# Kernel tuning notes

Hardware: AMD Instinct MI355X
Metric: run time of the kernel (lower is better)

Reference implementation:

```python
import itertools
import jax, jax.numpy as jnp
import numpy as np

# ---- constant tables / bases ----
Y_TABLE_NP = np.array([
    [16, 11, 10, 16, 24, 40, 51, 61],
    [12, 12, 14, 19, 26, 58, 60, 55],
    [14, 13, 16, 24, 40, 57, 69, 56],
    [14, 17, 22, 29, 51, 87, 80, 62],
    [18, 22, 37, 56, 68, 109, 103, 77],
    [24, 35, 55, 64, 81, 104, 113, 92],
    [49, 64, 78, 87, 103, 121, 120, 101],
    [72, 92, 95, 98, 112, 100, 103, 99]], dtype=np.float32)
C_TABLE_NP = np.full((8, 8), 99, dtype=np.float32)
C_TABLE_NP[:4, :4] = np.array([[17, 18, 24, 47], [18, 21, 26, 66],
                               [24, 26, 56, 99], [47, 66, 99, 99]], dtype=np.float32)

def _bases():
    dct = np.zeros((8, 8, 8, 8), dtype=np.float32)
    idct = np.zeros((8, 8, 8, 8), dtype=np.float32)
    for x, y, u, v in itertools.product(range(8), repeat=4):
        dct[x, y, u, v] = np.cos((2 * x + 1) * u * np.pi / 16) * np.cos((2 * y + 1) * v * np.pi / 16)
        idct[x, y, u, v] = np.cos((2 * u + 1) * x * np.pi / 16) * np.cos((2 * v + 1) * y * np.pi / 16)
    alpha = np.array([1.0 / np.sqrt(2)] + [1.0] * 7, dtype=np.float32)
    ao = np.outer(alpha, alpha).astype(np.float32)
    return jnp.asarray(dct), jnp.asarray(ao * 0.25), jnp.asarray(idct), jnp.asarray(ao)

DCT_T, DCT_SCALE, IDCT_T, ALPHA = _bases()
FACTOR = 0.4  # quality_to_factor(80) = (200 - 2*80)/100


def diff_round(x):
    r = jnp.round(x)
    return r + (x - r) ** 3


def _blocks(img):  # (B,H,W) -> (B, H*W/64, 8, 8)
    B, H, W = img.shape
    return img.reshape(B, H // 8, 8, W // 8, 8).transpose(0, 1, 3, 2, 4).reshape(B, -1, 8, 8)


def _merge(patches, H, W):  # (B, N, 8, 8) -> (B, H, W)
    B = patches.shape[0]
    return patches.reshape(B, H // 8, W // 8, 8, 8).transpose(0, 1, 3, 2, 4).reshape(B, H, W)


def setup_inputs() -> dict:
    key = jax.random.key(0)
    image = jax.random.uniform(key, (32, 3, 512, 512), dtype=jnp.float32)
    return {"image": image,
            "y_table": jnp.asarray(Y_TABLE_NP),
            "c_table": jnp.asarray(C_TABLE_NP)}


def reference(image, y_table, c_table):
    B, _, H, W = image.shape
    x = image * 255.0
    # RGB -> YCbCr (matrix stored transposed in torch, tensordot over channel)
    rgb2ycc = jnp.array([[0.299, 0.587, 0.114],
                         [-0.168736, -0.331264, 0.5],
                         [0.5, -0.418688, -0.081312]], dtype=jnp.float32)
    shift = jnp.array([0.0, 128.0, 128.0], dtype=jnp.float32)
    ycc = jnp.einsum('bchw,kc->bhwk', x, rgb2ycc) + shift  # (B,H,W,3)
    y = ycc[..., 0]
    # chroma subsampling: 2x2 average pool
    def pool2(ch):
        return ch.reshape(B, H // 2, 2, W // 2, 2).mean(axis=(2, 4))
    cb = pool2(ycc[..., 1])
    cr = pool2(ycc[..., 2])

    def compress(ch, table):
        blk = _blocks(ch) - 128.0
        d = DCT_SCALE * jnp.einsum('bnxy,xyuv->bnuv', blk, DCT_T)
        return diff_round(d / (table * FACTOR))

    yq = compress(y, y_table)
    cbq = compress(cb, c_table)
    crq = compress(cr, c_table)

    def decompress(q, table, h, w):
        d = (q * (table * FACTOR)) * ALPHA
        blk = 0.25 * jnp.einsum('bnuv,uvxy->bnxy', d, IDCT_T) + 128.0
        return _merge(blk, h, w)

    y_rec = decompress(yq, y_table, H, W)
    cb_rec = decompress(cbq, c_table, H // 2, W // 2)
    cr_rec = decompress(crq, c_table, H // 2, W // 2)

    def up2(ch):
        b, h, w = ch.shape
        return jnp.broadcast_to(ch[:, :, None, :, None], (b, h, 2, w, 2)).reshape(b, 2 * h, 2 * w)

    ycc_rec = jnp.stack([y_rec, up2(cb_rec), up2(cr_rec)], axis=-1)  # (B,H,W,3)
    ycc2rgb = jnp.array([[1.0, 0.0, 1.402],
                         [1.0, -0.344136, -0.714136],
                         [1.0, 1.772, 0.0]], dtype=jnp.float32)
    shift2 = jnp.array([0.0, -128.0, -128.0], dtype=jnp.float32)
    rgb = jnp.einsum('bhwk,ck->bhwc', ycc_rec + shift2, ycc2rgb)
    rgb = rgb.transpose(0, 3, 1, 2)  # (B,3,H,W)
    return jnp.clip(rgb, 0.0, 255.0) / 255.0
```

## Files before the change

### kernel.cpp

```cpp
#include <hip/hip_runtime.h>
#include <math.h>

#define IMG_H 512
#define IMG_W 512
#define IMG_HW (IMG_H * IMG_W)

namespace {

constexpr float CFv[9] = {
    1.0f,
    0.98078528040323044913f,
    0.92387953251128675613f,
    0.83146961230254523708f,
    0.70710678118654752440f,
    0.55557023301960222474f,
    0.38268343236508977173f,
    0.19509032201612826785f,
    0.0f
};

struct CTab {
    float  cf[8][8];
    double cd[8][8];
    float  aof[8][8];
    float  scalef[8][8];
};

constexpr CTab make_ctab() {
    CTab t{};
    for (int y = 0; y < 8; y++) {
        for (int v = 0; v < 8; v++) {
            int a = ((2 * y + 1) * v) & 31;
            if (a > 16) a = 32 - a;
            float val = (a <= 8) ? CFv[a] : -CFv[16 - a];
            t.cf[y][v] = val;
            t.cd[y][v] = (double)val;
        }
    }
    constexpr float A0 = 0.70710678118654752440f;
    for (int u = 0; u < 8; u++) {
        for (int v = 0; v < 8; v++) {
            float au = (u == 0) ? A0 : 1.0f;
            float av = (v == 0) ? A0 : 1.0f;
            float ao = au * av;
            t.aof[u][v] = ao;
            t.scalef[u][v] = ao * 0.25f;
        }
    }
    return t;
}

constexpr CTab CT = make_ctab();

#define OFF_CBP 8448
#define OFF_CRP 10624
#define OFF_QY  12800
#define OFF_QC  13952
#define SMEM_BYTES 15104

__device__ __forceinline__ void xpose8_d(double v[8]) {
    const int l = threadIdx.x & 7;
    #pragma unroll
    for (int m = 1; m < 8; m <<= 1) {
        #pragma unroll
        for (int k = 0; k < 8; k++) {
            if ((k & m) == 0) {
                const int kp = k | m;
                double send = (l & m) ? v[k] : v[kp];
                double recv = __shfl_xor(send, m);
                v[k]  = (l & m) ? recv : v[k];
                v[kp] = (l & m) ? v[kp] : recv;
            }
        }
    }
}

__device__ __forceinline__ void xpose8_f(float v[8]) {
    const int l = threadIdx.x & 7;
    #pragma unroll
    for (int m = 1; m < 8; m <<= 1) {
        #pragma unroll
        for (int k = 0; k < 8; k++) {
            if ((k & m) == 0) {
                const int kp = k | m;
                float send = (l & m) ? v[k] : v[kp];
                float recv = __shfl_xor(send, m);
                v[k]  = (l & m) ? recv : v[k];
                v[kp] = (l & m) ? v[kp] : recv;
            }
        }
    }
}

}

__global__ void __launch_bounds__(256, 6) djpeg_kernel(
    const float* __restrict__ img,
    const float* __restrict__ ytab,
    const float* __restrict__ ctab,
    float* __restrict__ out)
{
    __shared__ __align__(16) unsigned char smem[SMEM_BYTES];
    double* lY  = (double*)(smem);
    double* cbP = (double*)(smem + OFF_CBP);
    double* crP = (double*)(smem + OFF_CRP);
    double* qY  = (double*)(smem + OFF_QY);
    double* qC  = (double*)(smem + OFF_QC);
    float* yR  = (float*)(smem);
    float* cbR = (float*)(smem + 4224);
    float* crR = (float*)(smem + 5312);

    const int t  = threadIdx.x;
    const int X0 = blockIdx.x * 64;
    const int Y0 = blockIdx.y * 16;
    const int bi = blockIdx.z;

    if (t < 128) {
        const float* tab = (t < 64) ? ytab : ctab;
        double* q = (t < 64) ? qY : qC;
        int e = t & 63, u = e >> 3, v = e & 7;
        float tfacf = tab[e] * 0.4f;
        double tf = (double)tfacf;
        q[v * 18 + 2 * u]     = (double)CT.scalef[u][v] / tf;
        q[v * 18 + 2 * u + 1] = tf * (double)CT.aof[u][v];
    }

    {
        const int x = t & 63, yb = t >> 6;
        double accb[2] = {0.0, 0.0}, accr[2] = {0.0, 0.0};
        size_t base = ((size_t)bi * 3) * IMG_HW + (size_t)Y0 * IMG_W + X0 + x;
        #pragma unroll
        for (int i = 0; i < 4; i++) {
            int y = yb * 4 + i;
            size_t p = base + (size_t)y * IMG_W;
            double R = (double)img[p] * 255.0;
            double G = (double)img[p + IMG_HW] * 255.0;
            double B = (double)img[p + 2 * IMG_HW] * 255.0;
            double Yv = (double)0.299f * R + (double)0.587f * G + (double)0.114f * B;
            double Cb = -(double)0.168736f * R - (double)0.331264f * G + (double)0.5f * B + 128.0;
            double Cr = (double)0.5f * R - (double)0.418688f * G - (double)0.081312f * B + 128.0;
            lY[y * 66 + x] = Yv;
            accb[i >> 1] += Cb;
            accr[i >> 1] += Cr;
        }
        #pragma unroll
        for (int p2 = 0; p2 < 2; p2++) {
            double hb = accb[p2] + __shfl_xor(accb[p2], 1);
            double hr = accr[p2] + __shfl_xor(accr[p2], 1);
            if ((x & 1) == 0) {
                int pr = yb * 2 + p2;
                cbP[pr * 34 + (x >> 1)] = hb * 0.25;
                crP[pr * 34 + (x >> 1)] = hr * 0.25;
            }
        }
    }
    __syncthreads();

    const bool act = (t < 192);
    const int r = t & 7;
    const double* src = lY;
    const double* qtab = qY;
    float* dstR = yR;
    if (act) {
        if (t < 128) {
            int g = t >> 3, by = g >> 3, bx = g & 7;
            src  = lY + (by * 8 + r) * 66 + bx * 8;
            dstR = yR + (by * 8 + r) * 66 + bx * 8;
            qtab = qY;
        } else {
            int c = t - 128;
            int isCr = c >> 5;
            int g2 = (c >> 3) & 3;
            src  = (isCr ? crP : cbP) + r * 34 + g2 * 8;
            dstR = (isCr ? crR : cbR) + r * 34 + g2 * 8;
            qtab = qC;
        }
    }

    double s1[8];
    if (act) {
        double a[8];
        #pragma unroll
        for (int y = 0; y < 8; y++) a[y] = src[y] - 128.0;
        #pragma unroll
        for (int v = 0; v < 8; v++) {
            double s = a[0] * CT.cd[0][v];
            #pragma unroll
            for (int y = 1; y < 8; y++) s += a[y] * CT.cd[y][v];
            s1[v] = s;
        }
        xpose8_d(s1);
    }

    float mrow[8];
    if (act) {
        float dq[8];
        #pragma unroll
        for (int u = 0; u < 8; u++) {
            double D = s1[0] * CT.cd[0][u];
            #pragma unroll
            for (int x = 1; x < 8; x++) D += s1[x] * CT.cd[x][u];
            double fs = qtab[r * 18 + 2 * u];
            double ds = qtab[r * 18 + 2 * u + 1];
            double xq = D * fs;
            double rq = rint(xq);
            double e  = xq - rq;
            dq[u] = (float)((rq + e * e * e) * ds);
        }
        #pragma unroll
        for (int x = 0; x < 8; x++) {
            float s = dq[0] * CT.cf[x][0];
            #pragma unroll
            for (int u = 1; u < 8; u++) s += dq[u] * CT.cf[x][u];
            mrow[x] = s;
        }
        xpose8_f(mrow);
    }

    __syncthreads();

    if (act) {
        #pragma unroll
        for (int y = 0; y < 8; y++) {
            float s = mrow[0] * CT.cf[y][0];
            #pragma unroll
            for (int v = 1; v < 8; v++) s += mrow[v] * CT.cf[y][v];
            dstR[y] = 0.25f * s + 128.0f;
        }
    }
    __syncthreads();

    {
        const int x = t & 63, yb = t >> 6;
        size_t base = ((size_t)bi * 3) * IMG_HW + (size_t)Y0 * IMG_W + X0 + x;
        #pragma unroll
        for (int i = 0; i < 4; i++) {
            int y = yb * 4 + i;
            float Yv = yR[y * 66 + x];
            float Cb = cbR[(y >> 1) * 34 + (x >> 1)] - 128.0f;
            float Cr = crR[(y >> 1) * 34 + (x >> 1)] - 128.0f;
            float Rr = Yv + 1.402f * Cr;
            float Gg = Yv - 0.344136f * Cb - 0.714136f * Cr;
            float Bb = Yv + 1.772f * Cb;
            Rr = fminf(fmaxf(Rr, 0.0f), 255.0f) * (1.0f / 255.0f);
            Gg = fminf(fmaxf(Gg, 0.0f), 255.0f) * (1.0f / 255.0f);
            Bb = fminf(fmaxf(Bb, 0.0f), 255.0f) * (1.0f / 255.0f);
            size_t p = base + (size_t)y * IMG_W;
            out[p] = Rr;
            out[p + IMG_HW] = Gg;
            out[p + 2 * IMG_HW] = Bb;
        }
    }
}

extern "C" void kernel_launch(void* const* d_in, const int* in_sizes, int n_in,
                              void* d_out, int out_size, void* d_ws, size_t ws_size,
                              hipStream_t stream) {
    (void)n_in; (void)out_size; (void)d_ws; (void)ws_size;
    const float* img = (const float*)d_in[0];
    const float* yt  = (const float*)d_in[1];
    const float* ct  = (const float*)d_in[2];
    float* out = (float*)d_out;
    int B = in_sizes[0] / (3 * IMG_HW);
    dim3 grid(IMG_W / 64, IMG_H / 16, B);
    djpeg_kernel<<<grid, dim3(256, 1, 1), 0, stream>>>(img, yt, ct, out);
}
```

Baseline: 183.5 us.

## Use butterfly DCT/IDCT, LDS transposes, and float4 vectorized global I/O

Replaces the naive 8x8 matrix-product DCT and IDCT with even/odd butterfly factorizations, cutting double-precision multiplies. Replaces the shuffle-based register transposes with transposes through shared memory. Switches global loads and stores and the LDS staging to float4/double2 vector accesses, with pitches changed to keep alignment. Part of the dequantization and cube rounding now runs in float instead of double, which trades some precision for cheaper arithmetic.

```diff
diff --git a/kernel.cpp b/kernel.cpp
--- a/kernel.cpp
+++ b/kernel.cpp
@@ -52,47 +52,48 @@
 
 constexpr CTab CT = make_ctab();
 
+__device__ __forceinline__ void fwd8_d(const double a[8], double s[8]) {
+    double e0 = a[0] + a[7], e1 = a[1] + a[6], e2 = a[2] + a[5], e3 = a[3] + a[4];
+    double o0 = a[0] - a[7], o1 = a[1] - a[6], o2 = a[2] - a[5], o3 = a[3] - a[4];
+    double ee0 = e0 + e3, ee1 = e1 + e2, eo0 = e0 - e3, eo1 = e1 - e2;
+    s[0] = ee0 + ee1;
+    s[4] = (ee0 - ee1) * CT.cd[0][4];
+    s[2] = eo0 * CT.cd[0][2] + eo1 * CT.cd[1][2];
+    s[6] = eo0 * CT.cd[0][6] + eo1 * CT.cd[1][6];
+    #pragma unroll
+    for (int k = 0; k < 4; k++) {
+        const int v = 2 * k + 1;
+        s[v] = o0 * CT.cd[0][v] + o1 * CT.cd[1][v] + o2 * CT.cd[2][v] + o3 * CT.cd[3][v];
+    }
+}
+
+__device__ __forceinline__ void inv8_f(const float d[8], float m[8]) {
+    float eea = fmaf(CT.cf[0][4], d[4], d[0]);
+    float eeb = fmaf(CT.cf[1][4], d[4], d[0]);
+    float u2a = d[2] * CT.cf[0][2] + d[6] * CT.cf[0][6];
+    float u2b = d[2] * CT.cf[1][2] + d[6] * CT.cf[1][6];
+    float E0 = eea + u2a, E1 = eeb + u2b, E2 = eeb - u2b, E3 = eea - u2a;
+    float O0 = d[1] * CT.cf[0][1] + d[3] * CT.cf[0][3] + d[5] * CT.cf[0][5] + d[7] * CT.cf[0][7];
+    float O1 = d[1] * CT.cf[1][1] + d[3] * CT.cf[1][3] + d[5] * CT.cf[1][5] + d[7] * CT.cf[1][7];
+    float O2 = d[1] * CT.cf[2][1] + d[3] * CT.cf[2][3] + d[5] * CT.cf[2][5] + d[7] * CT.cf[2][7];
+    float O3 = d[1] * CT.cf[3][1] + d[3] * CT.cf[3][3] + d[5] * CT.cf[3][5] + d[7] * CT.cf[3][7];
+    m[0] = E0 + O0; m[7] = E0 - O0;
+    m[1] = E1 + O1; m[6] = E1 - O1;
+    m[2] = E2 + O2; m[5] = E2 - O2;
+    m[3] = E3 + O3; m[4] = E3 - O3;
+}
+
+}
+
 #define OFF_CBP 8448
 #define OFF_CRP 10624
-#define OFF_QY  12800
-#define OFF_QC  13952
-#define SMEM_BYTES 15104
-
-__device__ __forceinline__ void xpose8_d(double v[8]) {
-    const int l = threadIdx.x & 7;
-    #pragma unroll
-    for (int m = 1; m < 8; m <<= 1) {
-        #pragma unroll
-        for (int k = 0; k < 8; k++) {
-            if ((k & m) == 0) {
-                const int kp = k | m;
-                double send = (l & m) ? v[k] : v[kp];
-                double recv = __shfl_xor(send, m);
-                v[k]  = (l & m) ? recv : v[k];
-                v[kp] = (l & m) ? v[kp] : recv;
-            }
-        }
-    }
-}
-
-__device__ __forceinline__ void xpose8_f(float v[8]) {
-    const int l = threadIdx.x & 7;
-    #pragma unroll
-    for (int m = 1; m < 8; m <<= 1) {
-        #pragma unroll
-        for (int k = 0; k < 8; k++) {
-            if ((k & m) == 0) {
-                const int kp = k | m;
-                float send = (l & m) ? v[k] : v[kp];
-                float recv = __shfl_xor(send, m);
-                v[k]  = (l & m) ? recv : v[k];
-                v[kp] = (l & m) ? v[kp] : recv;
-            }
-        }
-    }
-}
-
-}
+#define OFF_QYF 12800
+#define OFF_QCF 13440
+#define OFF_DSY 14080
+#define OFF_DSC 14464
+#define OFF_CBR 4352
+#define OFF_CRR 5504
+#define SMEM_BYTES 14848
 
 __global__ void __launch_bounds__(256, 6) djpeg_kernel(
     const float* __restrict__ img,
@@ -101,14 +102,16 @@
     float* __restrict__ out)
 {
     __shared__ __align__(16) unsigned char smem[SMEM_BYTES];
-    double* lY  = (double*)(smem);
-    double* cbP = (double*)(smem + OFF_CBP);
-    double* crP = (double*)(smem + OFF_CRP);
-    double* qY  = (double*)(smem + OFF_QY);
-    double* qC  = (double*)(smem + OFF_QC);
-    float* yR  = (float*)(smem);
-    float* cbR = (float*)(smem + 4224);
-    float* crR = (float*)(smem + 5312);
+    double* lY   = (double*)(smem);
+    double* cbP  = (double*)(smem + OFF_CBP);
+    double* crP  = (double*)(smem + OFF_CRP);
+    double* qYfs = (double*)(smem + OFF_QYF);
+    double* qCfs = (double*)(smem + OFF_QCF);
+    float*  dsY  = (float*)(smem + OFF_DSY);
+    float*  dsC  = (float*)(smem + OFF_DSC);
+    float*  yR   = (float*)(smem);
+    float*  cbR  = (float*)(smem + OFF_CBR);
+    float*  crR  = (float*)(smem + OFF_CRR);
 
     const int t  = threadIdx.x;
     const int X0 = blockIdx.x * 64;
@@ -117,139 +120,158 @@
 
     if (t < 128) {
         const float* tab = (t < 64) ? ytab : ctab;
-        double* q = (t < 64) ? qY : qC;
+        double* qf = (t < 64) ? qYfs : qCfs;
+        float*  df = (t < 64) ? dsY : dsC;
         int e = t & 63, u = e >> 3, v = e & 7;
         float tfacf = tab[e] * 0.4f;
         double tf = (double)tfacf;
-        q[v * 18 + 2 * u]     = (double)CT.scalef[u][v] / tf;
-        q[v * 18 + 2 * u + 1] = tf * (double)CT.aof[u][v];
+        qf[v * 10 + u] = (double)CT.scalef[u][v] / tf;
+        df[v * 12 + u] = (float)(tf * (double)CT.aof[u][v]);
     }
 
     {
-        const int x = t & 63, yb = t >> 6;
-        double accb[2] = {0.0, 0.0}, accr[2] = {0.0, 0.0};
-        size_t base = ((size_t)bi * 3) * IMG_HW + (size_t)Y0 * IMG_W + X0 + x;
+        const int xq = t & 15, yb = t >> 4;
+        size_t base = ((size_t)bi * 3) * IMG_HW + (size_t)(Y0 + yb) * IMG_W + X0 + xq * 4;
+        const float4 rf = *(const float4*)(img + base);
+        const float4 gf = *(const float4*)(img + base + IMG_HW);
+        const float4 bf = *(const float4*)(img + base + 2 * IMG_HW);
+        const double kYR =  (double)0.299f    * 255.0, kYG =  (double)0.587f    * 255.0, kYB =  (double)0.114f    * 255.0;
+        const double kbR = -(double)0.168736f * 255.0, kbG = -(double)0.331264f * 255.0, kbB =  (double)0.5f      * 255.0;
+        const double krR =  (double)0.5f      * 255.0, krG = -(double)0.418688f * 255.0, krB = -(double)0.081312f * 255.0;
+        const float rr[4] = {rf.x, rf.y, rf.z, rf.w};
+        const float gg[4] = {gf.x, gf.y, gf.z, gf.w};
+        const float bb[4] = {bf.x, bf.y, bf.z, bf.w};
+        double Yv[4], Cbv[4], Crv[4];
         #pragma unroll
         for (int i = 0; i < 4; i++) {
-            int y = yb * 4 + i;
-            size_t p = base + (size_t)y * IMG_W;
-            double R = (double)img[p] * 255.0;
-            double G = (double)img[p + IMG_HW] * 255.0;
-            double B = (double)img[p + 2 * IMG_HW] * 255.0;
-            double Yv = (double)0.299f * R + (double)0.587f * G + (double)0.114f * B;
-            double Cb = -(double)0.168736f * R - (double)0.331264f * G + (double)0.5f * B + 128.0;
-            double Cr = (double)0.5f * R - (double)0.418688f * G - (double)0.081312f * B + 128.0;
-            lY[y * 66 + x] = Yv;
-            accb[i >> 1] += Cb;
-            accr[i >> 1] += Cr;
-        }
-        #pragma unroll
-        for (int p2 = 0; p2 < 2; p2++) {
-            double hb = accb[p2] + __shfl_xor(accb[p2], 1);
-            double hr = accr[p2] + __shfl_xor(accr[p2], 1);
-            if ((x & 1) == 0) {
-                int pr = yb * 2 + p2;
-                cbP[pr * 34 + (x >> 1)] = hb * 0.25;
-                crP[pr * 34 + (x >> 1)] = hr * 0.25;
-            }
+            double R = (double)rr[i], G = (double)gg[i], B = (double)bb[i];
+            Yv[i]  = kYR * R + kYG * G + kYB * B;
+            Cbv[i] = kbR * R + kbG * G + kbB * B + 128.0;
+            Crv[i] = krR * R + krG * G + krB * B + 128.0;
+        }
+        double2* yw = (double2*)(lY + yb * 66 + xq * 4);
+        yw[0] = make_double2(Yv[0], Yv[1]);
+        yw[1] = make_double2(Yv[2], Yv[3]);
+        double cb0 = Cbv[0] + Cbv[1], cb1 = Cbv[2] + Cbv[3];
+        double cr0 = Crv[0] + Crv[1], cr1 = Crv[2] + Crv[3];
+        cb0 += __shfl_xor(cb0, 16);
+        cb1 += __shfl_xor(cb1, 16);
+        cr0 += __shfl_xor(cr0, 16);
+        cr1 += __shfl_xor(cr1, 16);
+        if ((yb & 1) == 0) {
+            int pr = yb >> 1;
+            *(double2*)(cbP + pr * 34 + xq * 2) = make_double2(cb0 * 0.25, cb1 * 0.25);
+            *(double2*)(crP + pr * 34 + xq * 2) = make_double2(cr0 * 0.25, cr1 * 0.25);
         }
     }
     __syncthreads();
 
     const bool act = (t < 192);
     const int r = t & 7;
-    const double* src = lY;
-    const double* qtab = qY;
-    float* dstR = yR;
+    double* blkd = lY;  const double* qfp = qYfs;  const float* dfp = dsY;
+    float*  blkf = yR;
+    int sD = 66, sF = 68;
+    if (t < 128) {
+        int g = t >> 3, by = g >> 3, bx = g & 7;
+        blkd = lY + (by * 8) * 66 + bx * 8;
+        blkf = yR + (by * 8) * 68 + bx * 8;
+    } else if (t < 192) {
+        int c = t - 128, isCr = c >> 5, g2 = (c >> 3) & 3;
+        blkd = (isCr ? crP : cbP) + g2 * 8;
+        blkf = (isCr ? crR : cbR) + g2 * 8;
+        qfp = qCfs; dfp = dsC;
+        sD = 34; sF = 36;
+    }
+
+    float dq[8];
     if (act) {
-        if (t < 128) {
-            int g = t >> 3, by = g >> 3, bx = g & 7;
-            src  = lY + (by * 8 + r) * 66 + bx * 8;
-            dstR = yR + (by * 8 + r) * 66 + bx * 8;
-            qtab = qY;
-        } else {
-            int c = t - 128;
-            int isCr = c >> 5;
-            int g2 = (c >> 3) & 3;
-            src  = (isCr ? crP : cbP) + r * 34 + g2 * 8;
-            dstR = (isCr ? crR : cbR) + r * 34 + g2 * 8;
-            qtab = qC;
-        }
-    }
-
-    double s1[8];
+        const double* sp = blkd + r * sD;
+        const double2 a01 = *(const double2*)(sp + 0);
+        const double2 a23 = *(const double2*)(sp + 2);
+        const double2 a45 = *(const double2*)(sp + 4);
+        const double2 a67 = *(const double2*)(sp + 6);
+        const double a[8] = {a01.x, a01.y, a23.x, a23.y, a45.x, a45.y, a67.x, a67.y};
+        double s1[8];
+        fwd8_d(a, s1);
+        s1[0] -= 1024.0;
+
+        #pragma unroll
+        for (int v = 0; v < 8; v++) blkd[v * sD + r] = s1[v];
+        asm volatile("s_waitcnt lgkmcnt(0)" ::: "memory");
+        const double* rp = blkd + r * sD;
+        const double2 b01 = *(const double2*)(rp + 0);
+        const double2 b23 = *(const double2*)(rp + 2);
+        const double2 b45 = *(const double2*)(rp + 4);
+        const double2 b67 = *(const double2*)(rp + 6);
+        const double s2[8] = {b01.x, b01.y, b23.x, b23.y, b45.x, b45.y, b67.x, b67.y};
+
+        double D[8];
+        fwd8_d(s2, D);
+        const double2 f01 = *(const double2*)(qfp + r * 10 + 0);
+        const double2 f23 = *(const double2*)(qfp + r * 10 + 2);
+        const double2 f45 = *(const double2*)(qfp + r * 10 + 4);
+        const double2 f67 = *(const double2*)(qfp + r * 10 + 6);
+        const double fsv[8] = {f01.x, f01.y, f23.x, f23.y, f45.x, f45.y, f67.x, f67.y};
+        const float4 dA = *(const float4*)(dfp + r * 12);
+        const float4 dB = *(const float4*)(dfp + r * 12 + 4);
+        const float dsv[8] = {dA.x, dA.y, dA.z, dA.w, dB.x, dB.y, dB.z, dB.w};
+        #pragma unroll
+        for (int u = 0; u < 8; u++) {
+            double xq = D[u] * fsv[u];
+            double rq = rint(xq);
+            float ef  = (float)(xq - rq);
+            float rqf = (float)rq;
+            dq[u] = (rqf + ef * ef * ef) * dsv[u];
+        }
+    }
+
+    __syncthreads();
+
     if (act) {
-        double a[8];
-        #pragma unroll
-        for (int y = 0; y < 8; y++) a[y] = src[y] - 128.0;
-        #pragma unroll
-        for (int v = 0; v < 8; v++) {
-            double s = a[0] * CT.cd[0][v];
-            #pragma unroll
-            for (int y = 1; y < 8; y++) s += a[y] * CT.cd[y][v];
-            s1[v] = s;
-        }
-        xpose8_d(s1);
-    }
-
-    float mrow[8];
-    if (act) {
-        float dq[8];
-        #pragma unroll
-        for (int u = 0; u < 8; u++) {
-            double D = s1[0] * CT.cd[0][u];
-            #pragma unroll
-            for (int x = 1; x < 8; x++) D += s1[x] * CT.cd[x][u];
-            double fs = qtab[r * 18 + 2 * u];
-            double ds = qtab[r * 18 + 2 * u + 1];
-            double xq = D * fs;
-            double rq = rint(xq);
-            double e  = xq - rq;
-            dq[u] = (float)((rq + e * e * e) * ds);
-        }
-        #pragma unroll
-        for (int x = 0; x < 8; x++) {
-            float s = dq[0] * CT.cf[x][0];
-            #pragma unroll
-            for (int u = 1; u < 8; u++) s += dq[u] * CT.cf[x][u];
-            mrow[x] = s;
-        }
-        xpose8_f(mrow);
-    }
-
+        float mc[8];
+        inv8_f(dq, mc);
+
+        #pragma unroll
+        for (int p = 0; p < 8; p++) blkf[p * sF + r] = mc[p];
+        asm volatile("s_waitcnt lgkmcnt(0)" ::: "memory");
+        const float* fp_ = blkf + r * sF;
+        const float4 m0 = *(const float4*)(fp_);
+        const float4 m1 = *(const float4*)(fp_ + 4);
+        const float mrow[8] = {m0.x, m0.y, m0.z, m0.w, m1.x, m1.y, m1.z, m1.w};
+
+        float px[8];
+        inv8_f(mrow, px);
+        float* fw = blkf + r * sF;
+        *(float4*)(fw)     = make_float4(fmaf(0.25f, px[0], 128.0f), fmaf(0.25f, px[1], 128.0f),
+                                         fmaf(0.25f, px[2], 128.0f), fmaf(0.25f, px[3], 128.0f));
+        *(float4*)(fw + 4) = make_float4(fmaf(0.25f, px[4], 128.0f), fmaf(0.25f, px[5], 128.0f),
+                                         fmaf(0.25f, px[6], 128.0f), fmaf(0.25f, px[7], 128.0f));
+    }
     __syncthreads();
 
-    if (act) {
-        #pragma unroll
-        for (int y = 0; y < 8; y++) {
-            float s = mrow[0] * CT.cf[y][0];
-            #pragma unroll
-            for (int v = 1; v < 8; v++) s += mrow[v] * CT.cf[y][v];
-            dstR[y] = 0.25f * s + 128.0f;
-        }
-    }
-    __syncthreads();
-
     {
-        const int x = t & 63, yb = t >> 6;
-        size_t base = ((size_t)bi * 3) * IMG_HW + (size_t)Y0 * IMG_W + X0 + x;
+        const int xq = t & 15, yb = t >> 4;
+        const float4 yv  = *(const float4*)(yR + yb * 68 + xq * 4);
+        const float2 cbv = *(const float2*)(cbR + (yb >> 1) * 36 + xq * 2);
+        const float2 crv = *(const float2*)(crR + (yb >> 1) * 36 + xq * 2);
+        const float yy[4]  = {yv.x, yv.y, yv.z, yv.w};
+        const float cbs[2] = {cbv.x - 128.0f, cbv.y - 128.0f};
+        const float crs[2] = {crv.x - 128.0f, crv.y - 128.0f};
+        float R4[4], G4[4], B4[4];
         #pragma unroll
         for (int i = 0; i < 4; i++) {
-            int y = yb * 4 + i;
-            float Yv = yR[y * 66 + x];
-            float Cb = cbR[(y >> 1) * 34 + (x >> 1)] - 128.0f;
-            float Cr = crR[(y >> 1) * 34 + (x >> 1)] - 128.0f;
+            float Yv = yy[i], Cb = cbs[i >> 1], Cr = crs[i >> 1];
             float Rr = Yv + 1.402f * Cr;
             float Gg = Yv - 0.344136f * Cb - 0.714136f * Cr;
             float Bb = Yv + 1.772f * Cb;
-            Rr = fminf(fmaxf(Rr, 0.0f), 255.0f) * (1.0f / 255.0f);
-            Gg = fminf(fmaxf(Gg, 0.0f), 255.0f) * (1.0f / 255.0f);
-            Bb = fminf(fmaxf(Bb, 0.0f), 255.0f) * (1.0f / 255.0f);
-            size_t p = base + (size_t)y * IMG_W;
-            out[p] = Rr;
-            out[p + IMG_HW] = Gg;
-            out[p + 2 * IMG_HW] = Bb;
-        }
+            R4[i] = fminf(fmaxf(Rr, 0.0f), 255.0f) * (1.0f / 255.0f);
+            G4[i] = fminf(fmaxf(Gg, 0.0f), 255.0f) * (1.0f / 255.0f);
+            B4[i] = fminf(fmaxf(Bb, 0.0f), 255.0f) * (1.0f / 255.0f);
+        }
+        size_t base = ((size_t)bi * 3) * IMG_HW + (size_t)(Y0 + yb) * IMG_W + X0 + xq * 4;
+        *(float4*)(out + base)              = make_float4(R4[0], R4[1], R4[2], R4[3]);
+        *(float4*)(out + base + IMG_HW)     = make_float4(G4[0], G4[1], G4[2], G4[3]);
+        *(float4*)(out + base + 2 * IMG_HW) = make_float4(B4[0], B4[1], B4[2], B4[3]);
     }
 }
 
```

Measured after the change: 181.6 us. Within noise of the previous version (-1.0%).
